# Optimization experiments

Hardware: AMD Instinct MI355X
Metric: run time of the kernel (lower is better)

Reference implementation:

```python
import jax, jax.numpy as jnp
import numpy as np

B, T = 2, 2048
D_MODEL, D_HIDDEN = 1024, 2048
N_EXPERTS, TOP_K = 8, 2
N_TOKENS = B * T
CAPACITY = 2 * N_TOKENS * TOP_K // N_EXPERTS  # 4096


def setup_inputs() -> dict:
    key = jax.random.key(0)
    k_x, k_rw, k_w, k_v, k_o = jax.random.split(key, 5)
    x = jax.random.normal(k_x, (B, T, D_MODEL), jnp.float32)
    # router: nn.Linear(d_model, n_experts) -> weight [E, D], bias [E]
    router_w = jax.random.normal(k_rw, (N_EXPERTS, D_MODEL), jnp.float32) * D_MODEL ** -0.5
    router_b = jnp.zeros((N_EXPERTS,), jnp.float32)
    # stacked expert params, matching SwiGLU init scales
    W = jax.random.normal(k_w, (N_EXPERTS, D_MODEL, D_HIDDEN), jnp.float32) * D_MODEL ** -0.5
    V = jax.random.normal(k_v, (N_EXPERTS, D_MODEL, D_HIDDEN), jnp.float32) * D_MODEL ** -0.5
    W_out = jax.random.normal(k_o, (N_EXPERTS, D_HIDDEN, D_MODEL), jnp.float32) * D_HIDDEN ** -0.5
    return {"x": x, "router_w": router_w, "router_b": router_b, "W": W, "V": V, "W_out": W_out}


def reference(x, router_w, router_b, W, V, W_out):
    Bq, Tq, D = x.shape
    N = Bq * Tq
    x_flat = x.reshape(N, D)

    # token-level top-k routing
    router_logits = x_flat @ router_w.T + router_b            # [N, E]
    top_vals, top_ids = jax.lax.top_k(router_logits, TOP_K)   # [N, K]
    top_probs = jax.nn.softmax(top_vals, axis=-1)             # [N, K]

    # pad row N: gathers with fill index N read zeros / contribute zero weight
    x_pad = jnp.concatenate([x_flat, jnp.zeros((1, D), x_flat.dtype)], axis=0)
    probs_pad = jnp.concatenate([top_probs, jnp.zeros((1, TOP_K), top_probs.dtype)], axis=0)

    out = jnp.zeros((N + 1, D), x_flat.dtype)
    for e in range(N_EXPERTS):  # static small loop over experts
        tok, slot = jnp.nonzero(top_ids == e, size=CAPACITY, fill_value=(N, 0))
        w = probs_pad[tok, slot][:, None]     # [C, 1], zero for padding slots
        xin = x_pad[tok]                      # [C, D] gather
        a = xin @ W[e]                        # [C, H]
        b = xin @ V[e]                        # [C, H]
        y = (a * (b * jax.nn.sigmoid(b))) @ W_out[e]  # SwiGLU: a * swish(b) -> [C, D]
        out = out.at[tok].add(y * w)          # weighted scatter-add
    return out[:N].reshape(Bq, Tq, D)
```

## Files before the change

### kernel.cpp

```cpp
#include <hip/hip_runtime.h>
#include <cstdint>
#include <cstddef>

#define N_TOK 4096
#define DM    1024
#define DH    2048
#define NE    8
#define NSLOT 8192

typedef short bf16x8_t __attribute__((ext_vector_type(8)));
typedef float f32x4    __attribute__((ext_vector_type(4)));
typedef unsigned short u16x8 __attribute__((ext_vector_type(8)));

__device__ __forceinline__ unsigned short f2bf(float f) {
  union { float f; unsigned int u; } v; v.f = f;
  unsigned int u = v.u;
  u += 0x7fffu + ((u >> 16) & 1u);
  return (unsigned short)(u >> 16);
}

#define GLD16(gp, lp)                                                          \
  __builtin_amdgcn_global_load_lds(                                            \
      (const __attribute__((address_space(1))) void*)(gp),                     \
      (__attribute__((address_space(3))) void*)(lp), 16, 0, 0)

__device__ __forceinline__ int expert_off(const int* __restrict__ counts, int e, int* cnt) {
  int off = 0, s = 0;
#pragma unroll
  for (int i = 0; i < NE; i++) { if (i == e) off = s; s += counts[i]; }
  *cnt = counts[e];
  return off;
}

__global__ __launch_bounds__(256) void k_transpose(
    const float* __restrict__ W, const float* __restrict__ V,
    const float* __restrict__ Wout, unsigned short* __restrict__ B1t,
    unsigned short* __restrict__ B2t, int* __restrict__ counts) {
  if (blockIdx.z == 0 && blockIdx.x == 0 && blockIdx.y == 0 && threadIdx.x < NE)
    counts[threadIdx.x] = 0;

  const int z = blockIdx.z;
  const float* s;
  unsigned short* d;
  int R, C, xt, yt;
  if (z < 16) {
    const int e = z & 7;
    s = ((z < 8) ? W : V) + (size_t)e * DM * DH;
    d = B1t + (size_t)e * 4096 * DM + (size_t)((z < 8) ? 0 : DH) * DM;
    R = DM; C = DH; xt = blockIdx.x; yt = blockIdx.y;
  } else {
    const int e = z - 16;
    s = Wout + (size_t)e * DH * DM;
    d = B2t + (size_t)e * DM * DH;
    R = DH; C = DM;
    const int flat = blockIdx.x * 16 + blockIdx.y;
    xt = flat & 15; yt = flat >> 4;
  }
  const int c0 = xt * 64, r0 = yt * 64;
  __shared__ float tile[64][65];
  const int t = threadIdx.x;
  {
    const int cc = (t & 15) * 4;
#pragma unroll
    for (int j = 0; j < 4; j++) {
      const int r = (t >> 4) + j * 16;
      const float4 v = *(const float4*)(s + (size_t)(r0 + r) * C + c0 + cc);
      tile[r][cc + 0] = v.x; tile[r][cc + 1] = v.y;
      tile[r][cc + 2] = v.z; tile[r][cc + 3] = v.w;
    }
  }
  __syncthreads();
  {
    const int r8 = (t & 7) * 8;
#pragma unroll
    for (int j = 0; j < 2; j++) {
      const int c = (t >> 3) + j * 32;
      u16x8 o;
#pragma unroll
      for (int i = 0; i < 8; i++) o[i] = f2bf(tile[r8 + i][c]);
      *(u16x8*)(d + (size_t)(c0 + c) * R + r0 + r8) = o;
    }
  }
}

__global__ __launch_bounds__(256) void k_router(
    const float* __restrict__ x, const float* __restrict__ rw,
    const float* __restrict__ rb, int* __restrict__ counts,
    int* __restrict__ meta_e, int* __restrict__ meta_idx,
    float* __restrict__ meta_p) {
  const int wv = threadIdx.x >> 6;
  const int l  = threadIdx.x & 63;
  const int tk = blockIdx.x * 4 + wv;
  const float* xr = x + (size_t)tk * DM;

  float acc[NE];
#pragma unroll
  for (int e = 0; e < NE; e++) acc[e] = 0.f;
#pragma unroll 4
  for (int i = 0; i < DM / 64; i++) {
    const float xv = xr[i * 64 + l];
#pragma unroll
    for (int e = 0; e < NE; e++) acc[e] += xv * rw[e * DM + i * 64 + l];
  }
#pragma unroll
  for (int off = 32; off > 0; off >>= 1) {
#pragma unroll
    for (int e = 0; e < NE; e++) acc[e] += __shfl_xor(acc[e], off);
  }
#pragma unroll
  for (int e = 0; e < NE; e++) acc[e] += rb[e];

  float v0 = -1e30f; int e0 = 0;
#pragma unroll
  for (int e = 0; e < NE; e++) { if (acc[e] > v0) { v0 = acc[e]; e0 = e; } }
  float v1 = -1e30f; int e1 = 0;
#pragma unroll
  for (int e = 0; e < NE; e++) { if (e != e0 && acc[e] > v1) { v1 = acc[e]; e1 = e; } }
  const float p0 = 1.0f / (1.0f + __expf(v1 - v0));
  const float p1 = 1.0f - p0;

  if (l == 0) {
    const int i0 = atomicAdd(&counts[e0], 1);
    const int i1 = atomicAdd(&counts[e1], 1);
    meta_e[tk * 2 + 0] = e0;  meta_e[tk * 2 + 1] = e1;
    meta_idx[tk * 2 + 0] = i0; meta_idx[tk * 2 + 1] = i1;
    meta_p[tk * 2 + 0] = p0;  meta_p[tk * 2 + 1] = p1;
  }
}

__global__ __launch_bounds__(256) void k_gather(
    const float* __restrict__ x, const int* __restrict__ meta_e,
    const int* __restrict__ meta_idx, const int* __restrict__ counts,
    unsigned short* __restrict__ Xg) {
  const int tk = blockIdx.x;
  int offs[NE];
  { int s = 0;
#pragma unroll
    for (int e = 0; e < NE; e++) { offs[e] = s; s += counts[e]; } }
  const int s0 = tk * 2, s1 = s0 + 1;
  const int g0 = offs[meta_e[s0]] + meta_idx[s0];
  const int g1 = offs[meta_e[s1]] + meta_idx[s1];
  const float4 v = ((const float4*)(x + (size_t)tk * DM))[threadIdx.x];
  ushort4 o;
  o.x = f2bf(v.x); o.y = f2bf(v.y); o.z = f2bf(v.z); o.w = f2bf(v.w);
  *(ushort4*)(Xg + (size_t)g0 * DM + threadIdx.x * 4) = o;
  *(ushort4*)(Xg + (size_t)g1 * DM + threadIdx.x * 4) = o;
}

__global__ __launch_bounds__(256, 2) void k_gemm1(
    const unsigned short* __restrict__ Xg, const unsigned short* __restrict__ B1t,
    unsigned short* __restrict__ G, const int* __restrict__ counts) {
  const int e = blockIdx.z;
  int cnt;
  const int off = expert_off(counts, e, &cnt);
  const int mt = blockIdx.y;
  if (mt * 128 >= cnt) return;
  const int h0 = blockIdx.x * 128;
  const int row_base = off + mt * 128;

  __shared__ unsigned short As[128 * 32];
  __shared__ unsigned short Ws[128 * 32];
  __shared__ unsigned short Vs[128 * 32];

  const int t = threadIdx.x;
  const int l = t & 63;
  const int w = t >> 6;
  const int wm = (w >> 1) * 64;
  const int wn = (w & 1) * 64;
  const int lr = l & 15;
  const int kq = (l >> 4) * 8;

  const unsigned short* Bw = B1t + ((size_t)e * 4096 + h0) * DM;
  const unsigned short* Bv = Bw + (size_t)DH * DM;

  const int c0 = t, c1 = t + 256;
  const int ar0 = c0 >> 2, ak0 = (c0 & 3) * 8;
  const int ar1 = c1 >> 2, ak1 = (c1 & 3) * 8;
  const int arow0 = min(row_base + ar0, NSLOT - 1);
  const int arow1 = min(row_base + ar1, NSLOT - 1);

  f32x4 acc_a[4][4], acc_b[4][4];
  const f32x4 z4 = {0.f, 0.f, 0.f, 0.f};
#pragma unroll
  for (int i = 0; i < 4; i++)
#pragma unroll
    for (int j = 0; j < 4; j++) { acc_a[i][j] = z4; acc_b[i][j] = z4; }

  for (int k0 = 0; k0 < DM; k0 += 32) {
    __syncthreads();
    GLD16(Xg + (size_t)arow0 * DM + k0 + ak0, As + c0 * 8);
    GLD16(Xg + (size_t)arow1 * DM + k0 + ak1, As + c1 * 8);
    GLD16(Bw + (size_t)ar0 * DM + k0 + ak0, Ws + c0 * 8);
    GLD16(Bw + (size_t)ar1 * DM + k0 + ak1, Ws + c1 * 8);
    GLD16(Bv + (size_t)ar0 * DM + k0 + ak0, Vs + c0 * 8);
    GLD16(Bv + (size_t)ar1 * DM + k0 + ak1, Vs + c1 * 8);
    __syncthreads();

    bf16x8_t af[4], wf[4], vf[4];
#pragma unroll
    for (int mi = 0; mi < 4; mi++)
      af[mi] = *(const bf16x8_t*)&As[(wm + mi * 16 + lr) * 32 + kq];
#pragma unroll
    for (int ni = 0; ni < 4; ni++) {
      wf[ni] = *(const bf16x8_t*)&Ws[(wn + ni * 16 + lr) * 32 + kq];
      vf[ni] = *(const bf16x8_t*)&Vs[(wn + ni * 16 + lr) * 32 + kq];
    }
#pragma unroll
    for (int mi = 0; mi < 4; mi++)
#pragma unroll
      for (int ni = 0; ni < 4; ni++) {
        acc_a[mi][ni] = __builtin_amdgcn_mfma_f32_16x16x32_bf16(af[mi], wf[ni], acc_a[mi][ni], 0, 0, 0);
        acc_b[mi][ni] = __builtin_amdgcn_mfma_f32_16x16x32_bf16(af[mi], vf[ni], acc_b[mi][ni], 0, 0, 0);
      }
  }

  const int q4 = (l >> 4) * 4;
#pragma unroll
  for (int mi = 0; mi < 4; mi++) {
#pragma unroll
    for (int r = 0; r < 4; r++) {
      const int mloc = mt * 128 + wm + mi * 16 + q4 + r;
      if (mloc >= cnt) continue;
      unsigned short* grow = G + (size_t)(off + mloc) * DH;
#pragma unroll
      for (int ni = 0; ni < 4; ni++) {
        const int h = h0 + wn + ni * 16 + lr;
        const float a = acc_a[mi][ni][r];
        const float b = acc_b[mi][ni][r];
        const float s = b / (1.0f + __expf(-b));
        grow[h] = f2bf(a * s);
      }
    }
  }
}

__global__ __launch_bounds__(256, 2) void k_gemm2(
    const unsigned short* __restrict__ G, const unsigned short* __restrict__ B2t,
    float* __restrict__ Y, const int* __restrict__ counts) {
  const int z = blockIdx.z;
  const int e = z & 7;
  const int half = z >> 3;
  int cnt;
  const int off = expert_off(counts, e, &cnt);
  const int mt = blockIdx.y;
  if (mt * 128 >= cnt) return;
  const int n0 = blockIdx.x * 128;
  const int row_base = off + mt * 128;
  const int kbase = half * 1024;

  __shared__ unsigned short As[128 * 32];
  __shared__ unsigned short Bs[128 * 32];

  const int t = threadIdx.x;
  const int l = t & 63;
  const int w = t >> 6;
  const int wm = (w >> 1) * 64;
  const int wn = (w & 1) * 64;
  const int lr = l & 15;
  const int kq = (l >> 4) * 8;

  const unsigned short* Bp = B2t + ((size_t)e * DM + n0) * DH;

  const int c0 = t, c1 = t + 256;
  const int ar0 = c0 >> 2, ak0 = (c0 & 3) * 8;
  const int ar1 = c1 >> 2, ak1 = (c1 & 3) * 8;
  const int arow0 = min(row_base + ar0, NSLOT - 1);
  const int arow1 = min(row_base + ar1, NSLOT - 1);

  f32x4 acc[4][4];
  const f32x4 z4 = {0.f, 0.f, 0.f, 0.f};
#pragma unroll
  for (int i = 0; i < 4; i++)
#pragma unroll
    for (int j = 0; j < 4; j++) acc[i][j] = z4;

  for (int kk = 0; kk < 1024; kk += 32) {
    const int k0 = kbase + kk;
    __syncthreads();
    GLD16(G + (size_t)arow0 * DH + k0 + ak0, As + c0 * 8);
    GLD16(G + (size_t)arow1 * DH + k0 + ak1, As + c1 * 8);
    GLD16(Bp + (size_t)ar0 * DH + k0 + ak0, Bs + c0 * 8);
    GLD16(Bp + (size_t)ar1 * DH + k0 + ak1, Bs + c1 * 8);
    __syncthreads();

    bf16x8_t af[4], bf[4];
#pragma unroll
    for (int mi = 0; mi < 4; mi++)
      af[mi] = *(const bf16x8_t*)&As[(wm + mi * 16 + lr) * 32 + kq];
#pragma unroll
    for (int ni = 0; ni < 4; ni++)
      bf[ni] = *(const bf16x8_t*)&Bs[(wn + ni * 16 + lr) * 32 + kq];
#pragma unroll
    for (int mi = 0; mi < 4; mi++)
#pragma unroll
      for (int ni = 0; ni < 4; ni++)
        acc[mi][ni] = __builtin_amdgcn_mfma_f32_16x16x32_bf16(af[mi], bf[ni], acc[mi][ni], 0, 0, 0);
  }

  float* Yh = Y + (size_t)half * NSLOT * DM;
  const int q4 = (l >> 4) * 4;
#pragma unroll
  for (int mi = 0; mi < 4; mi++) {
#pragma unroll
    for (int r = 0; r < 4; r++) {
      const int mloc = mt * 128 + wm + mi * 16 + q4 + r;
      if (mloc >= cnt) continue;
      float* yrow = Yh + (size_t)(off + mloc) * DM;
#pragma unroll
      for (int ni = 0; ni < 4; ni++)
        yrow[n0 + wn + ni * 16 + lr] = acc[mi][ni][r];
    }
  }
}

__global__ __launch_bounds__(256) void k_combine(
    const float* __restrict__ Y, const int* __restrict__ meta_e,
    const int* __restrict__ meta_idx, const float* __restrict__ meta_p,
    const int* __restrict__ counts, float* __restrict__ out) {
  const int tk = blockIdx.x;
  int offs[NE];
  { int s = 0;
#pragma unroll
    for (int e = 0; e < NE; e++) { offs[e] = s; s += counts[e]; } }
  const int s0 = tk * 2, s1 = s0 + 1;
  const int g0 = offs[meta_e[s0]] + meta_idx[s0];
  const int g1 = offs[meta_e[s1]] + meta_idx[s1];
  const float w0 = meta_p[s0], w1 = meta_p[s1];
  const float* Y1 = Y + (size_t)NSLOT * DM;
  const float4 a0 = ((const float4*)(Y  + (size_t)g0 * DM))[threadIdx.x];
  const float4 a1 = ((const float4*)(Y1 + (size_t)g0 * DM))[threadIdx.x];
  const float4 b0 = ((const float4*)(Y  + (size_t)g1 * DM))[threadIdx.x];
  const float4 b1 = ((const float4*)(Y1 + (size_t)g1 * DM))[threadIdx.x];
  float4 o;
  o.x = w0 * (a0.x + a1.x) + w1 * (b0.x + b1.x);
  o.y = w0 * (a0.y + a1.y) + w1 * (b0.y + b1.y);
  o.z = w0 * (a0.z + a1.z) + w1 * (b0.z + b1.z);
  o.w = w0 * (a0.w + a1.w) + w1 * (b0.w + b1.w);
  ((float4*)(out + (size_t)tk * DM))[threadIdx.x] = o;
}

extern "C" void kernel_launch(void* const* d_in, const int* in_sizes, int n_in,
                              void* d_out, int out_size, void* d_ws, size_t ws_size,
                              hipStream_t stream) {
  const float* x    = (const float*)d_in[0];
  const float* rw   = (const float*)d_in[1];
  const float* rb   = (const float*)d_in[2];
  const float* W    = (const float*)d_in[3];
  const float* V    = (const float*)d_in[4];
  const float* Wout = (const float*)d_in[5];
  float* out = (float*)d_out;

  char* p = (char*)d_ws;
  unsigned short* B1t = (unsigned short*)p; p += (size_t)NE * 4096 * DM * 2;
  float*          Y   = (float*)B1t;
  unsigned short* B2t = (unsigned short*)p; p += (size_t)NE * DM * DH * 2;
  unsigned short* Xg  = (unsigned short*)p; p += (size_t)NSLOT * DM * 2;
  unsigned short* G   = (unsigned short*)p; p += (size_t)NSLOT * DH * 2;
  int*   counts      = (int*)p;   p += 256;
  int*   meta_e      = (int*)p;   p += (size_t)N_TOK * 2 * 4;
  int*   meta_idx    = (int*)p;   p += (size_t)N_TOK * 2 * 4;
  float* meta_p      = (float*)p; p += (size_t)N_TOK * 2 * 4;

  k_transpose<<<dim3(32, 16, 24), 256, 0, stream>>>(W, V, Wout, B1t, B2t, counts);
  k_router<<<N_TOK / 4, 256, 0, stream>>>(x, rw, rb, counts, meta_e, meta_idx, meta_p);
  k_gather<<<N_TOK, 256, 0, stream>>>(x, meta_e, meta_idx, counts, Xg);
  k_gemm1<<<dim3(DH / 128, NSLOT / 128, NE), 256, 0, stream>>>(Xg, B1t, G, counts);
  k_gemm2<<<dim3(DM / 128, NSLOT / 128, 2 * NE), 256, 0, stream>>>(G, B2t, Y, counts);
  k_combine<<<N_TOK, 256, 0, stream>>>(Y, meta_e, meta_idx, meta_p, counts, out);
}
```

Baseline: 516.2 us.

## Double K-step per barrier in expert GEMMs and store partial outputs as bf16

Both expert GEMM kernels now load two 32-wide K slices per synchronisation round into doubled shared buffers, halving the number of barrier pairs per tile. The second GEMM also writes its split-K partial results in bf16 instead of fp32, and the combine kernel reads and widens them, cutting partial-output write and read traffic in half. The cost is double the shared memory per block, which may lower occupancy, and extra rounding of partial sums before the final fp32 combine.

```diff
diff --git a/kernel.cpp b/kernel.cpp
--- a/kernel.cpp
+++ b/kernel.cpp
@@ -17,6 +17,11 @@
   unsigned int u = v.u;
   u += 0x7fffu + ((u >> 16) & 1u);
   return (unsigned short)(u >> 16);
+}
+
+__device__ __forceinline__ float bf2f(unsigned short h) {
+  union { unsigned int u; float f; } v; v.u = ((unsigned int)h) << 16;
+  return v.f;
 }
 
 #define GLD16(gp, lp)                                                          \
@@ -158,9 +163,9 @@
   const int h0 = blockIdx.x * 128;
   const int row_base = off + mt * 128;
 
-  __shared__ unsigned short As[128 * 32];
-  __shared__ unsigned short Ws[128 * 32];
-  __shared__ unsigned short Vs[128 * 32];
+  __shared__ unsigned short As[2][128 * 32];
+  __shared__ unsigned short Ws[2][128 * 32];
+  __shared__ unsigned short Vs[2][128 * 32];
 
   const int t = threadIdx.x;
   const int l = t & 63;
@@ -186,32 +191,41 @@
 #pragma unroll
     for (int j = 0; j < 4; j++) { acc_a[i][j] = z4; acc_b[i][j] = z4; }
 
-  for (int k0 = 0; k0 < DM; k0 += 32) {
+  for (int k0 = 0; k0 < DM; k0 += 64) {
     __syncthreads();
-    GLD16(Xg + (size_t)arow0 * DM + k0 + ak0, As + c0 * 8);
-    GLD16(Xg + (size_t)arow1 * DM + k0 + ak1, As + c1 * 8);
-    GLD16(Bw + (size_t)ar0 * DM + k0 + ak0, Ws + c0 * 8);
-    GLD16(Bw + (size_t)ar1 * DM + k0 + ak1, Ws + c1 * 8);
-    GLD16(Bv + (size_t)ar0 * DM + k0 + ak0, Vs + c0 * 8);
-    GLD16(Bv + (size_t)ar1 * DM + k0 + ak1, Vs + c1 * 8);
+    GLD16(Xg + (size_t)arow0 * DM + k0 + ak0,      &As[0][c0 * 8]);
+    GLD16(Xg + (size_t)arow1 * DM + k0 + ak1,      &As[0][c1 * 8]);
+    GLD16(Xg + (size_t)arow0 * DM + k0 + 32 + ak0, &As[1][c0 * 8]);
+    GLD16(Xg + (size_t)arow1 * DM + k0 + 32 + ak1, &As[1][c1 * 8]);
+    GLD16(Bw + (size_t)ar0 * DM + k0 + ak0,        &Ws[0][c0 * 8]);
+    GLD16(Bw + (size_t)ar1 * DM + k0 + ak1,        &Ws[0][c1 * 8]);
+    GLD16(Bw + (size_t)ar0 * DM + k0 + 32 + ak0,   &Ws[1][c0 * 8]);
+    GLD16(Bw + (size_t)ar1 * DM + k0 + 32 + ak1,   &Ws[1][c1 * 8]);
+    GLD16(Bv + (size_t)ar0 * DM + k0 + ak0,        &Vs[0][c0 * 8]);
+    GLD16(Bv + (size_t)ar1 * DM + k0 + ak1,        &Vs[0][c1 * 8]);
+    GLD16(Bv + (size_t)ar0 * DM + k0 + 32 + ak0,   &Vs[1][c0 * 8]);
+    GLD16(Bv + (size_t)ar1 * DM + k0 + 32 + ak1,   &Vs[1][c1 * 8]);
     __syncthreads();
 
-    bf16x8_t af[4], wf[4], vf[4];
-#pragma unroll
-    for (int mi = 0; mi < 4; mi++)
-      af[mi] = *(const bf16x8_t*)&As[(wm + mi * 16 + lr) * 32 + kq];
-#pragma unroll
-    for (int ni = 0; ni < 4; ni++) {
-      wf[ni] = *(const bf16x8_t*)&Ws[(wn + ni * 16 + lr) * 32 + kq];
-      vf[ni] = *(const bf16x8_t*)&Vs[(wn + ni * 16 + lr) * 32 + kq];
-    }
-#pragma unroll
-    for (int mi = 0; mi < 4; mi++)
+#pragma unroll
+    for (int ks = 0; ks < 2; ks++) {
+      bf16x8_t af[4], wf[4], vf[4];
+#pragma unroll
+      for (int mi = 0; mi < 4; mi++)
+        af[mi] = *(const bf16x8_t*)&As[ks][(wm + mi * 16 + lr) * 32 + kq];
 #pragma unroll
       for (int ni = 0; ni < 4; ni++) {
-        acc_a[mi][ni] = __builtin_amdgcn_mfma_f32_16x16x32_bf16(af[mi], wf[ni], acc_a[mi][ni], 0, 0, 0);
-        acc_b[mi][ni] = __builtin_amdgcn_mfma_f32_16x16x32_bf16(af[mi], vf[ni], acc_b[mi][ni], 0, 0, 0);
+        wf[ni] = *(const bf16x8_t*)&Ws[ks][(wn + ni * 16 + lr) * 32 + kq];
+        vf[ni] = *(const bf16x8_t*)&Vs[ks][(wn + ni * 16 + lr) * 32 + kq];
       }
+#pragma unroll
+      for (int mi = 0; mi < 4; mi++)
+#pragma unroll
+        for (int ni = 0; ni < 4; ni++) {
+          acc_a[mi][ni] = __builtin_amdgcn_mfma_f32_16x16x32_bf16(af[mi], wf[ni], acc_a[mi][ni], 0, 0, 0);
+          acc_b[mi][ni] = __builtin_amdgcn_mfma_f32_16x16x32_bf16(af[mi], vf[ni], acc_b[mi][ni], 0, 0, 0);
+        }
+    }
   }
 
   const int q4 = (l >> 4) * 4;
@@ -236,7 +250,7 @@
 
 __global__ __launch_bounds__(256, 2) void k_gemm2(
     const unsigned short* __restrict__ G, const unsigned short* __restrict__ B2t,
-    float* __restrict__ Y, const int* __restrict__ counts) {
+    unsigned short* __restrict__ Y, const int* __restrict__ counts) {
   const int z = blockIdx.z;
   const int e = z & 7;
   const int half = z >> 3;
@@ -248,8 +262,8 @@
   const int row_base = off + mt * 128;
   const int kbase = half * 1024;
 
-  __shared__ unsigned short As[128 * 32];
-  __shared__ unsigned short Bs[128 * 32];
+  __shared__ unsigned short As[2][128 * 32];
+  __shared__ unsigned short Bs[2][128 * 32];
 
   const int t = threadIdx.x;
   const int l = t & 63;
@@ -274,30 +288,37 @@
 #pragma unroll
     for (int j = 0; j < 4; j++) acc[i][j] = z4;
 
-  for (int kk = 0; kk < 1024; kk += 32) {
+  for (int kk = 0; kk < 1024; kk += 64) {
     const int k0 = kbase + kk;
     __syncthreads();
-    GLD16(G + (size_t)arow0 * DH + k0 + ak0, As + c0 * 8);
-    GLD16(G + (size_t)arow1 * DH + k0 + ak1, As + c1 * 8);
-    GLD16(Bp + (size_t)ar0 * DH + k0 + ak0, Bs + c0 * 8);
-    GLD16(Bp + (size_t)ar1 * DH + k0 + ak1, Bs + c1 * 8);
+    GLD16(G + (size_t)arow0 * DH + k0 + ak0,      &As[0][c0 * 8]);
+    GLD16(G + (size_t)arow1 * DH + k0 + ak1,      &As[0][c1 * 8]);
+    GLD16(G + (size_t)arow0 * DH + k0 + 32 + ak0, &As[1][c0 * 8]);
+    GLD16(G + (size_t)arow1 * DH + k0 + 32 + ak1, &As[1][c1 * 8]);
+    GLD16(Bp + (size_t)ar0 * DH + k0 + ak0,       &Bs[0][c0 * 8]);
+    GLD16(Bp + (size_t)ar1 * DH + k0 + ak1,       &Bs[0][c1 * 8]);
+    GLD16(Bp + (size_t)ar0 * DH + k0 + 32 + ak0,  &Bs[1][c0 * 8]);
+    GLD16(Bp + (size_t)ar1 * DH + k0 + 32 + ak1,  &Bs[1][c1 * 8]);
     __syncthreads();
 
-    bf16x8_t af[4], bf[4];
-#pragma unroll
-    for (int mi = 0; mi < 4; mi++)
-      af[mi] = *(const bf16x8_t*)&As[(wm + mi * 16 + lr) * 32 + kq];
-#pragma unroll
-    for (int ni = 0; ni < 4; ni++)
-      bf[ni] = *(const bf16x8_t*)&Bs[(wn + ni * 16 + lr) * 32 + kq];
-#pragma unroll
-    for (int mi = 0; mi < 4; mi++)
+#pragma unroll
+    for (int ks = 0; ks < 2; ks++) {
+      bf16x8_t af[4], bf[4];
+#pragma unroll
+      for (int mi = 0; mi < 4; mi++)
+        af[mi] = *(const bf16x8_t*)&As[ks][(wm + mi * 16 + lr) * 32 + kq];
 #pragma unroll
       for (int ni = 0; ni < 4; ni++)
-        acc[mi][ni] = __builtin_amdgcn_mfma_f32_16x16x32_bf16(af[mi], bf[ni], acc[mi][ni], 0, 0, 0);
-  }
-
-  float* Yh = Y + (size_t)half * NSLOT * DM;
+        bf[ni] = *(const bf16x8_t*)&Bs[ks][(wn + ni * 16 + lr) * 32 + kq];
+#pragma unroll
+      for (int mi = 0; mi < 4; mi++)
+#pragma unroll
+        for (int ni = 0; ni < 4; ni++)
+          acc[mi][ni] = __builtin_amdgcn_mfma_f32_16x16x32_bf16(af[mi], bf[ni], acc[mi][ni], 0, 0, 0);
+    }
+  }
+
+  unsigned short* Yh = Y + (size_t)half * NSLOT * DM;
   const int q4 = (l >> 4) * 4;
 #pragma unroll
   for (int mi = 0; mi < 4; mi++) {
@@ -305,16 +326,16 @@
     for (int r = 0; r < 4; r++) {
       const int mloc = mt * 128 + wm + mi * 16 + q4 + r;
       if (mloc >= cnt) continue;
-      float* yrow = Yh + (size_t)(off + mloc) * DM;
+      unsigned short* yrow = Yh + (size_t)(off + mloc) * DM;
 #pragma unroll
       for (int ni = 0; ni < 4; ni++)
-        yrow[n0 + wn + ni * 16 + lr] = acc[mi][ni][r];
+        yrow[n0 + wn + ni * 16 + lr] = f2bf(acc[mi][ni][r]);
     }
   }
 }
 
 __global__ __launch_bounds__(256) void k_combine(
-    const float* __restrict__ Y, const int* __restrict__ meta_e,
+    const unsigned short* __restrict__ Y, const int* __restrict__ meta_e,
     const int* __restrict__ meta_idx, const float* __restrict__ meta_p,
     const int* __restrict__ counts, float* __restrict__ out) {
   const int tk = blockIdx.x;
@@ -326,16 +347,16 @@
   const int g0 = offs[meta_e[s0]] + meta_idx[s0];
   const int g1 = offs[meta_e[s1]] + meta_idx[s1];
   const float w0 = meta_p[s0], w1 = meta_p[s1];
-  const float* Y1 = Y + (size_t)NSLOT * DM;
-  const float4 a0 = ((const float4*)(Y  + (size_t)g0 * DM))[threadIdx.x];
-  const float4 a1 = ((const float4*)(Y1 + (size_t)g0 * DM))[threadIdx.x];
-  const float4 b0 = ((const float4*)(Y  + (size_t)g1 * DM))[threadIdx.x];
-  const float4 b1 = ((const float4*)(Y1 + (size_t)g1 * DM))[threadIdx.x];
+  const unsigned short* Y1 = Y + (size_t)NSLOT * DM;
+  const ushort4 a0 = ((const ushort4*)(Y  + (size_t)g0 * DM))[threadIdx.x];
+  const ushort4 a1 = ((const ushort4*)(Y1 + (size_t)g0 * DM))[threadIdx.x];
+  const ushort4 b0 = ((const ushort4*)(Y  + (size_t)g1 * DM))[threadIdx.x];
+  const ushort4 b1 = ((const ushort4*)(Y1 + (size_t)g1 * DM))[threadIdx.x];
   float4 o;
-  o.x = w0 * (a0.x + a1.x) + w1 * (b0.x + b1.x);
-  o.y = w0 * (a0.y + a1.y) + w1 * (b0.y + b1.y);
-  o.z = w0 * (a0.z + a1.z) + w1 * (b0.z + b1.z);
-  o.w = w0 * (a0.w + a1.w) + w1 * (b0.w + b1.w);
+  o.x = w0 * (bf2f(a0.x) + bf2f(a1.x)) + w1 * (bf2f(b0.x) + bf2f(b1.x));
+  o.y = w0 * (bf2f(a0.y) + bf2f(a1.y)) + w1 * (bf2f(b0.y) + bf2f(b1.y));
+  o.z = w0 * (bf2f(a0.z) + bf2f(a1.z)) + w1 * (bf2f(b0.z) + bf2f(b1.z));
+  o.w = w0 * (bf2f(a0.w) + bf2f(a1.w)) + w1 * (bf2f(b0.w) + bf2f(b1.w));
   ((float4*)(out + (size_t)tk * DM))[threadIdx.x] = o;
 }
 
@@ -352,7 +373,7 @@
 
   char* p = (char*)d_ws;
   unsigned short* B1t = (unsigned short*)p; p += (size_t)NE * 4096 * DM * 2;
-  float*          Y   = (float*)B1t;
+  unsigned short* Y   = (unsigned short*)B1t;
   unsigned short* B2t = (unsigned short*)p; p += (size_t)NE * DM * DH * 2;
   unsigned short* Xg  = (unsigned short*)p; p += (size_t)NSLOT * DM * 2;
   unsigned short* G   = (unsigned short*)p; p += (size_t)NSLOT * DH * 2;
```

Measured after the change: 492.9 us. 4.5% less time.
